# Optimization experiments

Hardware: AMD Instinct MI355X
Metric: run time of the kernel (lower is better)

Reference implementation:

```python
import jax, jax.numpy as jnp
import numpy as np
from jax import lax

LB, UB = 0.0, 0.1
N_ITERS = 32  # fixed-point iterations for water-filling rebalance


def _conv(x, w, b):
    y = lax.conv_general_dilated(x, w, (1, 1), ((1, 1), (1, 1)),
                                 dimension_numbers=("NCHW", "OIHW", "NCHW"))
    return y + b[None, :, None, None]


def _maxpool2(x):
    return lax.reduce_window(x, -jnp.inf, lax.max, (1, 1, 2, 2), (1, 1, 2, 2), "VALID")


def _linear(x, w, b):
    return x @ w.T + b


def _gru(x_num, W_ih, W_hh, b_ih, b_hh):
    # x_num: [B, S, N]; torch GRU gate order r, z, n
    B = x_num.shape[0]
    H = W_hh.shape[1]
    xs = jnp.swapaxes(x_num, 0, 1)  # [S, B, N]

    def step(h, x_t):
        gi = x_t @ W_ih.T + b_ih            # [B, 3H]
        gh = h @ W_hh.T + b_hh              # [B, 3H]
        i_r, i_z, i_n = jnp.split(gi, 3, axis=-1)
        h_r, h_z, h_n = jnp.split(gh, 3, axis=-1)
        r = jax.nn.sigmoid(i_r + h_r)
        z = jax.nn.sigmoid(i_z + h_z)
        n = jnp.tanh(i_n + r * h_n)
        h_new = (1.0 - z) * n + z * h
        return h_new, None

    h0 = jnp.zeros((B, H), dtype=x_num.dtype)
    h_last, _ = lax.scan(step, h0, xs)
    return h_last


def _rebalance_one(w):
    # vectorized fixed-point version of the per-sample while-loop water-filling
    def body(carry, _):
        old, wc = carry
        leftover = jnp.sum(old - wc)
        mask = wc != UB
        s = jnp.sum(jnp.where(mask, wc, 0.0))
        gift = jnp.where(mask & (s > 0), leftover * wc / jnp.where(s > 0, s, 1.0), 0.0)
        new_old = wc + gift
        new_wc = jnp.clip(new_old, LB, UB)
        return (new_old, new_wc), None

    init = (w, jnp.clip(w, LB, UB))
    (_, wc), _ = lax.scan(body, init, None, length=N_ITERS)
    return wc


def setup_inputs() -> dict:
    key = jax.random.key(0)
    ks = jax.random.split(key, 16)
    B, S, N, H_IMG, W_IMG, HID = 16, 60, 50, 64, 60, 128
    fc_in = 64 * (H_IMG // 4) * (W_IMG // 4)  # 15360
    sc = 0.05
    return {
        "x_num": jax.random.normal(ks[0], (B, S, N), jnp.float32),
        "x_img": jax.random.uniform(ks[1], (B, N, H_IMG, W_IMG), jnp.float32),
        "conv1_w": jax.random.normal(ks[2], (32, 1, 3, 3), jnp.float32) * sc,
        "conv1_b": jnp.zeros((32,), jnp.float32),
        "conv2_w": jax.random.normal(ks[3], (64, 32, 3, 3), jnp.float32) * sc,
        "conv2_b": jnp.zeros((64,), jnp.float32),
        "fc1_w": jax.random.normal(ks[4], (64, fc_in), jnp.float32) * 0.01,
        "fc1_b": jnp.zeros((64,), jnp.float32),
        "fc_binary_w": jax.random.normal(ks[5], (1, 64), jnp.float32) * sc,
        "fc_binary_b": jnp.zeros((1,), jnp.float32),
        "fc2_w": jax.random.normal(ks[6], (128, 64), jnp.float32) * sc,
        "fc2_b": jnp.zeros((128,), jnp.float32),
        "W_ih": jax.random.normal(ks[7], (3 * HID, N), jnp.float32) * sc,
        "W_hh": jax.random.normal(ks[8], (3 * HID, HID), jnp.float32) * sc,
        "b_ih": jnp.zeros((3 * HID,), jnp.float32),
        "b_hh": jnp.zeros((3 * HID,), jnp.float32),
        "gru_fc_w": jax.random.normal(ks[9], (N, HID), jnp.float32) * sc,
        "gru_fc_b": jnp.zeros((N,), jnp.float32),
        "fusion_w": jax.random.normal(ks[10], (64, N + 128), jnp.float32) * sc,
        "fusion_b": jnp.zeros((64,), jnp.float32),
        "final_w": jax.random.normal(ks[11], (N, 64), jnp.float32) * sc,
        "final_b": jnp.zeros((N,), jnp.float32),
    }


def reference(x_num, x_img, conv1_w, conv1_b, conv2_w, conv2_b, fc1_w, fc1_b,
              fc_binary_w, fc_binary_b, fc2_w, fc2_b, W_ih, W_hh, b_ih, b_hh,
              gru_fc_w, gru_fc_b, fusion_w, fusion_b, final_w, final_b):
    B, S, N = x_num.shape
    # GRU branch: last hidden -> Linear -> [B, N]
    h_last = _gru(x_num, W_ih, W_hh, b_ih, b_hh)
    numerical_features = _linear(h_last, gru_fc_w, gru_fc_b)

    # CNN branch on per-stock chart images
    xi = x_img.reshape(B * N, 1, x_img.shape[2], x_img.shape[3])
    h = _maxpool2(jax.nn.relu(_conv(xi, conv1_w, conv1_b)))
    h = _maxpool2(jax.nn.relu(_conv(h, conv2_w, conv2_b)))
    h = h.reshape(B * N, -1)
    feats = jax.nn.relu(_linear(h, fc1_w, fc1_b))
    binary_pred = jax.nn.sigmoid(_linear(feats, fc_binary_w, fc_binary_b))
    cnn_features = _linear(feats, fc2_w, fc2_b).reshape(B, N, -1).mean(axis=1)

    fused = jax.nn.relu(_linear(jnp.concatenate([numerical_features, cnn_features], axis=1), fusion_w, fusion_b))
    w = jax.nn.softmax(_linear(fused, final_w, final_b), axis=1)
    portfolio_weights = jax.vmap(_rebalance_one)(w)
    return portfolio_weights, binary_pred.reshape(B, N)
```

## Files before the change

kernel.cpp:

```cpp
#include <hip/hip_runtime.h>
#include <hip/hip_bf16.h>
#include <hip/hip_fp16.h>

typedef unsigned short ushort_t;
typedef short short8_t __attribute__((ext_vector_type(8)));
typedef _Float16 half8_t __attribute__((ext_vector_type(8)));
typedef _Float16 h2 __attribute__((ext_vector_type(2)));
typedef float f32x4 __attribute__((ext_vector_type(4)));
typedef float f32x16 __attribute__((ext_vector_type(16)));
typedef ushort_t us4_t __attribute__((ext_vector_type(4)));

#define NBATCH 16
#define SEQ    60
#define NSTK   50
#define HID    128
#define G3     384
#define NIMG   800
#define IH     64
#define IW     60
#define P1H    32
#define P1W    30
#define P2C    64
#define FCIN   15360

#define OFF_WHHF   0u
#define OFF_WPREP  24576u
#define OFF_WFC1   33792u
#define OFF_GI     525312u
#define OFF_HLAST  893952u
#define OFF_POOL2  896000u
#define OFF_FC2O   7040000u
#define OFF_PART   7142400u
#define OFF_W1H    7961600u
#define WS_FLOATS  7961760u

#define E_WHH  49152
#define E_WPR  18432
#define E_FC1  983040
#define E_W1H  160
#define E_TOT  (E_WHH + E_WPR + E_FC1 + E_W1H)

struct __align__(16) ConvS {
    ushort_t pool1t[18][4][32][8];
    union {
        float    imgp[35][60];
        ushort_t pool2s[64][120];
    } u;
};
struct __align__(16) GruS {
    float    gh[16 * 388];
    ushort_t hb[16 * 136];
};
#define SMEM_BYTES 52224

__device__ __forceinline__ float fast_sig(float x) {
    const float e = __expf(-x);
    return __builtin_amdgcn_rcpf(1.f + e);
}
__device__ __forceinline__ float fast_tanh(float x) {
    const float xc = fmaxf(fminf(x, 15.f), -15.f);
    const float e = __expf(2.f * xc);
    return (e - 1.f) * __builtin_amdgcn_rcpf(e + 1.f);
}
__device__ __forceinline__ h2 hmax2v(h2 a, h2 b) {
    h2 r;
    r[0] = a[0] > b[0] ? a[0] : b[0];
    r[1] = a[1] > b[1] ? a[1] : b[1];
    return r;
}

__global__ __launch_bounds__(384) void k_pre(const float* __restrict__ xnum,
                                             const float* __restrict__ wih,
                                             const float* __restrict__ bih,
                                             const float* __restrict__ whh,
                                             const float* __restrict__ c2w,
                                             const float* __restrict__ fc1w,
                                             const float* __restrict__ c1w,
                                             const float* __restrict__ c1b,
                                             float* __restrict__ GI,
                                             ushort_t* __restrict__ whhf,
                                             ushort_t* __restrict__ wprep,
                                             ushort_t* __restrict__ wfc1,
                                             unsigned int* __restrict__ w1h)
{
    const int bid = blockIdx.x;
    if (bid < 960) {
        const int s = bid >> 4, b = bid & 15;
        const int j = threadIdx.x;
        const float* xr = xnum + (size_t)(b * SEQ + s) * NSTK;
        const float* wr = wih + (size_t)j * NSTK;
        float a = bih[j];
        #pragma unroll 10
        for (int k = 0; k < NSTK; ++k) a = fmaf(xr[k], wr[k], a);
        GI[((size_t)s * 16 + b) * G3 + j] = a;
        return;
    }
    const int idx = (bid - 960) * 384 + threadIdx.x;
    if (idx < E_WHH) {
        const int e = idx;
        const int i = e & 7, l = (e >> 3) & 63, ksj = e >> 9;
        const int ks = ksj & 3, jt = ksj >> 2;
        const int j = jt * 16 + (l & 15);
        const int k = ks * 32 + ((l >> 4) << 3) + i;
        __hip_bfloat16 hv = __float2bfloat16(whh[j * HID + k]);
        whhf[e] = *(ushort_t*)&hv;
    } else if (idx < E_WHH + E_WPR) {
        const int e = idx - E_WHH;
        const int i = e & 7, l = (e >> 3) & 63, rest = e >> 9;
        const int ks = rest & 1, mt = rest >> 1;
        const int tap = mt % 9, mm = mt / 9;
        const int oc = mm * 32 + (l & 31);
        const int ic = ks * 16 + ((l >> 5) << 3) + i;
        const _Float16 hv = (_Float16)c2w[((size_t)oc * 32 + ic) * 9 + tap];
        wprep[e] = *(const ushort_t*)&hv;
    } else if (idx < E_WHH + E_WPR + E_FC1) {
        const int e = idx - (E_WHH + E_WPR);
        const int i = e & 7, l = (e >> 3) & 63, rest = e >> 9;
        const int n = rest & 3, T = rest >> 2;
        const int oc = n * 16 + (l & 15);
        const int k = T * 32 + ((l >> 4) << 3) + i;
        __hip_bfloat16 hv = __float2bfloat16(fc1w[(size_t)oc * FCIN + k]);
        wfc1[e] = *(ushort_t*)&hv;
    } else if (idx < E_TOT) {
        const int e = idx - (E_WHH + E_WPR + E_FC1);
        if (e < 144) {
            const int p = e / 9, tap = e - p * 9;
            const int ch0 = (p >> 2) * 8 + (p & 3) * 2;
            const _Float16 lo = (_Float16)c1w[ch0 * 9 + tap];
            const _Float16 hi = (_Float16)c1w[(ch0 + 1) * 9 + tap];
            w1h[p * 9 + tap] = ((unsigned)*(const ushort_t*)&hi << 16) | *(const ushort_t*)&lo;
        } else {
            const int p = e - 144;
            const int ch0 = (p >> 2) * 8 + (p & 3) * 2;
            const _Float16 lo = (_Float16)c1b[ch0];
            const _Float16 hi = (_Float16)c1b[ch0 + 1];
            w1h[144 + p] = ((unsigned)*(const ushort_t*)&hi << 16) | *(const ushort_t*)&lo;
        }
    }
}

__global__ __launch_bounds__(512, 3) void k_mega(const float* __restrict__ x_img,
                                                 const unsigned int* __restrict__ w1h,
                                                 const float* __restrict__ c2b,
                                                 const ushort_t* __restrict__ wprep,
                                                 const float* __restrict__ GI,
                                                 const ushort_t* __restrict__ whhf,
                                                 const float* __restrict__ bhh,
                                                 ushort_t* __restrict__ pool2,
                                                 float* __restrict__ hlast)
{
    extern __shared__ char smraw[];
    const int tid = threadIdx.x;
    const int bid = blockIdx.x;

    if (bid == 0) {
        GruS* g = (GruS*)smraw;
        const int w = tid >> 6, l = tid & 63;
        const int arow = l & 15, kq = l >> 4;
        short8_t wfr[3][4];
        #pragma unroll
        for (int jj = 0; jj < 3; ++jj)
            #pragma unroll
            for (int ks = 0; ks < 4; ++ks)
                wfr[jj][ks] = *(const short8_t*)&whhf[((((w * 3 + jj) * 4 + ks) * 64 + l) * 8)];

        const int b = tid >> 5, hh0 = (tid & 31) * 4;
        const f32x4 bhr = *(const f32x4*)&bhh[hh0];
        const f32x4 bhz = *(const f32x4*)&bhh[128 + hh0];
        const f32x4 bhn = *(const f32x4*)&bhh[256 + hh0];
        float h0 = 0.f, h1 = 0.f, h2v = 0.f, h3 = 0.f;
        for (int i = tid; i < 1088; i += 512) ((unsigned int*)g->hb)[i] = 0u;
        const float* gi0 = GI + b * G3 + hh0;
        f32x4 cr = *(const f32x4*)(gi0);
        f32x4 cz = *(const f32x4*)(gi0 + 128);
        f32x4 cn = *(const f32x4*)(gi0 + 256);
        __syncthreads();

        for (int s = 0; s < SEQ; ++s) {
            const int sn = (s + 1 < SEQ) ? s + 1 : s;
            const float* gnx = GI + ((size_t)sn * 16 + b) * G3 + hh0;
            const f32x4 nr = *(const f32x4*)(gnx);
            const f32x4 nz = *(const f32x4*)(gnx + 128);
            const f32x4 nn = *(const f32x4*)(gnx + 256);

            #pragma unroll
            for (int jj = 0; jj < 3; ++jj) {
                f32x4 a = {0.f, 0.f, 0.f, 0.f};
                #pragma unroll
                for (int ks = 0; ks < 4; ++ks) {
                    short8_t af = *(const short8_t*)&g->hb[arow * 136 + ks * 32 + kq * 8];
                    a = __builtin_amdgcn_mfma_f32_16x16x32_bf16(af, wfr[jj][ks], a, 0, 0, 0);
                }
                const int jt = w * 3 + jj;
                #pragma unroll
                for (int r = 0; r < 4; ++r)
                    g->gh[(kq * 4 + r) * 388 + jt * 16 + arow] = a[r];
            }
            __syncthreads();

            const f32x4 gr = *(const f32x4*)&g->gh[b * 388 + hh0];
            const f32x4 gz = *(const f32x4*)&g->gh[b * 388 + 128 + hh0];
            const f32x4 gn = *(const f32x4*)&g->gh[b * 388 + 256 + hh0];
            float hv0, hv1, hv2, hv3;
            {
                const float r0 = fast_sig(cr[0] + gr[0] + bhr[0]);
                const float z0 = fast_sig(cz[0] + gz[0] + bhz[0]);
                const float n0 = fast_tanh(cn[0] + r0 * (gn[0] + bhn[0]));
                hv0 = (1.f - z0) * n0 + z0 * h0;
                const float r1 = fast_sig(cr[1] + gr[1] + bhr[1]);
                const float z1 = fast_sig(cz[1] + gz[1] + bhz[1]);
                const float n1 = fast_tanh(cn[1] + r1 * (gn[1] + bhn[1]));
                hv1 = (1.f - z1) * n1 + z1 * h1;
                const float r2 = fast_sig(cr[2] + gr[2] + bhr[2]);
                const float z2 = fast_sig(cz[2] + gz[2] + bhz[2]);
                const float n2 = fast_tanh(cn[2] + r2 * (gn[2] + bhn[2]));
                hv2 = (1.f - z2) * n2 + z2 * h2v;
                const float r3 = fast_sig(cr[3] + gr[3] + bhr[3]);
                const float z3 = fast_sig(cz[3] + gz[3] + bhz[3]);
                const float n3 = fast_tanh(cn[3] + r3 * (gn[3] + bhn[3]));
                hv3 = (1.f - z3) * n3 + z3 * h3;
            }
            h0 = hv0; h1 = hv1; h2v = hv2; h3 = hv3;
            us4_t hp;
            { __hip_bfloat16 t0 = __float2bfloat16(h0);  hp[0] = *(ushort_t*)&t0; }
            { __hip_bfloat16 t1 = __float2bfloat16(h1);  hp[1] = *(ushort_t*)&t1; }
            { __hip_bfloat16 t2 = __float2bfloat16(h2v); hp[2] = *(ushort_t*)&t2; }
            { __hip_bfloat16 t3 = __float2bfloat16(h3);  hp[3] = *(ushort_t*)&t3; }
            *(us4_t*)&g->hb[b * 136 + hh0] = hp;
            cr = nr; cz = nz; cn = nn;
            __syncthreads();
        }
        f32x4 ho = {h0, h1, h2v, h3};
        *(f32x4*)&hlast[b * HID + hh0] = ho;
        return;
    }

    ConvS* c = (ConvS*)smraw;
    const int img  = (bid - 1) >> 1;
    const int half = (bid - 1) & 1;
    const float* xim = x_img + (size_t)img * (IH * IW);
    const int rowbase = 29 * half;

    {
        const short8_t z = {0, 0, 0, 0, 0, 0, 0, 0};
        const int zrow = half ? 17 : 0;
        if (tid < 128) {
            const int cg = tid >> 5, xs = tid & 31;
            *(short8_t*)&c->pool1t[zrow][cg][xs][0] = z;
        } else if (tid < 272) {
            const int q = tid - 128;
            const int ly = q / 8, cg = (q >> 1) & 3, xs = (q & 1) * 31;
            *(short8_t*)&c->pool1t[ly][cg][xs][0] = z;
        }
    }
    {
        const f32x4* src = (const f32x4*)(xim + rowbase * IW);
        f32x4* dst = (f32x4*)c->u.imgp;
        for (int i = tid; i < 525; i += 512) dst[i] = src[i];
    }
    __syncthreads();

    if (tid < 510) {
        const int gj = tid / 30, px = tid - gj * 30;
        const int g = half * 15 + gj;
        const int ly = gj + 1 - half;
        const h2 z2 = {(_Float16)0.f, (_Float16)0.f};
        h2 patch2[4][4];
        #pragma unroll
        for (int yy = 0; yy < 4; ++yy) {
            const int giy = 2 * g - 1 + yy;
            const int liy = giy - rowbase;
            #pragma unroll
            for (int xx = 0; xx < 4; ++xx) {
                const int ix = 2 * px - 1 + xx;
                const float v = (giy >= 0 && giy < IH && ix >= 0 && ix < IW)
                                    ? c->u.imgp[liy][ix] : 0.f;
                const _Float16 vh = (_Float16)v;
                h2 p2; p2[0] = vh; p2[1] = vh;
                patch2[yy][xx] = p2;
            }
        }
        #pragma unroll
        for (int cg = 0; cg < 4; ++cg) {
            unsigned int ov[4];
            #pragma unroll
            for (int pr = 0; pr < 4; ++pr) {
                const int p = cg * 4 + pr;
                h2 wv[9];
                #pragma unroll
                for (int t = 0; t < 9; ++t) {
                    const unsigned int wu = w1h[p * 9 + t];
                    wv[t] = *(const h2*)&wu;
                }
                h2 a00 = z2, a01 = z2, a10 = z2, a11 = z2;
                #pragma unroll
                for (int ky = 0; ky < 3; ++ky)
                    #pragma unroll
                    for (int kx = 0; kx < 3; ++kx) {
                        const h2 wt = wv[ky * 3 + kx];
                        a00 = wt * patch2[ky][kx]     + a00;
                        a01 = wt * patch2[ky][kx + 1] + a01;
                        a10 = wt * patch2[ky + 1][kx] + a10;
                        a11 = wt * patch2[ky + 1][kx + 1] + a11;
                    }
                const unsigned int bu = w1h[144 + p];
                const h2 bia2 = *(const h2*)&bu;
                h2 m = hmax2v(hmax2v(a00, a01), hmax2v(a10, a11));
                h2 r = hmax2v(m + bia2, z2);
                ov[pr] = *(unsigned int*)&r;
            }
            *(uint4*)&c->pool1t[ly][cg][px + 1][0] = *(uint4*)ov;
        }
    }
    __syncthreads();

    {
        const int w  = tid >> 6, l = tid & 63;
        const int m  = w & 1;
        const int hi = l >> 5;
        const int col = l & 31;

        half8_t af[9][2];
        #pragma unroll
        for (int tap = 0; tap < 9; ++tap)
            #pragma unroll
            for (int ks = 0; ks < 2; ++ks)
                af[tap][ks] = *(const half8_t*)&wprep[(((m * 9 + tap) * 2 + ks) * 64 + l) * 8];
        float bia[16];
        #pragma unroll
        for (int r = 0; r < 16; ++r)
            bia[r] = c2b[m * 32 + (r & 3) + 8 * (r >> 2) + 4 * hi];

        const bool wr = ((col & 1) == 0) && (col < 30);
        const int px = col >> 1;

        #pragma unroll
        for (int yy = 0; yy < 2; ++yy) {
            const int ypl = (w >> 1) + yy * 4;
            f32x16 a0, a1;
            #pragma unroll
            for (int r = 0; r < 16; ++r) { a0[r] = 0.f; a1[r] = 0.f; }
            #pragma unroll
            for (int ro = 0; ro < 4; ++ro) {
                const int ly = 2 * ypl + ro;
                half8_t bf[3][2];
                #pragma unroll
                for (int kx = 0; kx < 3; ++kx)
                    #pragma unroll
                    for (int ks = 0; ks < 2; ++ks)
                        bf[kx][ks] = *(const half8_t*)&c->pool1t[ly][ks * 2 + hi][kx + col][0];
                if (ro < 3) {
                    #pragma unroll
                    for (int kx = 0; kx < 3; ++kx)
                        #pragma unroll
                        for (int ks = 0; ks < 2; ++ks)
                            a0 = __builtin_amdgcn_mfma_f32_32x32x16_f16(af[ro * 3 + kx][ks], bf[kx][ks], a0, 0, 0, 0);
                }
                if (ro >= 1) {
                    #pragma unroll
                    for (int kx = 0; kx < 3; ++kx)
                        #pragma unroll
                        for (int ks = 0; ks < 2; ++ks)
                            a1 = __builtin_amdgcn_mfma_f32_32x32x16_f16(af[(ro - 1) * 3 + kx][ks], bf[kx][ks], a1, 0, 0, 0);
                }
            }
            #pragma unroll
            for (int r = 0; r < 16; ++r) {
                float v = fmaxf(a0[r], a1[r]);
                v = fmaxf(v, __shfl_xor(v, 1, 64));
                v = fmaxf(v + bia[r], 0.f);
                if (wr) {
                    const int oc = m * 32 + (r & 3) + 8 * (r >> 2) + 4 * hi;
                    __hip_bfloat16 hv = __float2bfloat16(v);
                    c->u.pool2s[oc][ypl * 15 + px] = *(ushort_t*)&hv;
                }
            }
        }
        __syncthreads();
        {
            int4* dst = (int4*)(pool2 + (size_t)img * FCIN);
            const int4* src = (const int4*)c->u.pool2s;
            #pragma unroll
            for (int jj = 0; jj < 2; ++jj) {
                const int i = tid + jj * 512;
                if (i < 960) {
                    const int oc = i / 15, cc = i - oc * 15;
                    dst[oc * 30 + half * 15 + cc] = src[i];
                }
            }
        }
    }
}

__global__ __launch_bounds__(256) void k_fc1(const ushort_t* __restrict__ pool2,
                                             const ushort_t* __restrict__ wfc1,
                                             float* __restrict__ part)
{
    const int mt = blockIdx.x >> 4;
    const int ks = blockIdx.x & 15;
    const int n = threadIdx.x >> 6, l = threadIdx.x & 63;
    const int arow = l & 15, kq = l >> 4;
    const int img16 = mt * 16;
    const ushort_t* Ab = pool2 + (size_t)(img16 + arow) * FCIN + ks * 960 + kq * 8;
    const ushort_t* Bb = wfc1 + ((size_t)(ks * 30 * 4 + n) * 64 + l) * 8;
    f32x4 acc0 = {0.f, 0.f, 0.f, 0.f}, acc1 = {0.f, 0.f, 0.f, 0.f};
    #pragma unroll 10
    for (int t = 0; t < 30; t += 2) {
        const short8_t aA = *(const short8_t*)(Ab + (size_t)t * 32);
        const short8_t bA = *(const short8_t*)(Bb + (size_t)t * 2048);
        const short8_t aB = *(const short8_t*)(Ab + (size_t)(t + 1) * 32);
        const short8_t bB = *(const short8_t*)(Bb + (size_t)(t + 1) * 2048);
        acc0 = __builtin_amdgcn_mfma_f32_16x16x32_bf16(aA, bA, acc0, 0, 0, 0);
        acc1 = __builtin_amdgcn_mfma_f32_16x16x32_bf16(aB, bB, acc1, 0, 0, 0);
    }
    float* dst = &part[((size_t)ks * NIMG + img16 + kq * 4) * 64 + n * 16 + arow];
    #pragma unroll
    for (int r = 0; r < 4; ++r)
        dst[(size_t)r * 64] = acc0[r] + acc1[r];
}

__device__ __forceinline__ float wave_sum(float v) {
    #pragma unroll
    for (int o = 32; o > 0; o >>= 1) v += __shfl_xor(v, o, 64);
    return v;
}
__device__ __forceinline__ float wave_max(float v) {
    #pragma unroll
    for (int o = 32; o > 0; o >>= 1) v = fmaxf(v, __shfl_xor(v, o, 64));
    return v;
}

__global__ __launch_bounds__(512) void k_post(const float* __restrict__ part,
                                              const float* __restrict__ fc1b,
                                              const float* __restrict__ fbw,
                                              const float* __restrict__ fbb,
                                              const float* __restrict__ fc2w,
                                              const float* __restrict__ fc2b,
                                              float* __restrict__ out,
                                              float* __restrict__ fc2o)
{
    const int t = threadIdx.x;
    const int im8 = t >> 6;
    const int tl = t & 63;
    const int img = blockIdx.x * 8 + im8;
    float s = fc1b[tl];
    #pragma unroll
    for (int ks = 0; ks < 16; ++ks) s += part[((size_t)ks * NIMG + img) * 64 + tl];
    const float f = fmaxf(s, 0.f);
    __shared__ float flc[8][64];
    flc[im8][tl] = f;
    const float bs = wave_sum(f * fbw[tl]);
    if (tl == 0) out[800 + img] = 1.f / (1.f + expf(-(bs + fbb[0])));
    __syncthreads();
    #pragma unroll
    for (int q = 0; q < 2; ++q) {
        const int j = tl + q * 64;
        float a2 = fc2b[j];
        #pragma unroll 8
        for (int k = 0; k < 64; ++k) a2 = fmaf(flc[im8][k], fc2w[j * 64 + k], a2);
        fc2o[(size_t)img * 128 + j] = a2;
    }
}

__global__ __launch_bounds__(64) void k_final(const float* __restrict__ hlast,
                                              const float* __restrict__ fc2o,
                                              const float* __restrict__ gw,
                                              const float* __restrict__ gb,
                                              const float* __restrict__ fw,
                                              const float* __restrict__ fb,
                                              const float* __restrict__ finw,
                                              const float* __restrict__ finb,
                                              float* __restrict__ out)
{
    const int b = blockIdx.x, t = threadIdx.x;
    __shared__ float cf[128], nf[64], fu[64];
    #pragma unroll
    for (int jj = 0; jj < 2; ++jj) {
        const int j = t + jj * 64;
        float s = 0.f;
        for (int n = 0; n < NSTK; ++n) s += fc2o[(size_t)(b * NSTK + n) * 128 + j];
        cf[j] = s * (1.0f / 50.0f);
    }
    float s = 0.f;
    if (t < NSTK) {
        s = gb[t];
        for (int k = 0; k < HID; ++k) s = fmaf(hlast[b * HID + k], gw[t * HID + k], s);
    }
    nf[t] = (t < NSTK) ? s : 0.f;
    __syncthreads();
    float f = fb[t];
    for (int k = 0; k < NSTK; ++k) f = fmaf(nf[k], fw[t * 178 + k], f);
    for (int k = 0; k < 128; ++k) f = fmaf(cf[k], fw[t * 178 + 50 + k], f);
    fu[t] = fmaxf(f, 0.f);
    __syncthreads();
    float L = -3.4e38f;
    if (t < NSTK) {
        L = finb[t];
        for (int k = 0; k < 64; ++k) L = fmaf(fu[k], finw[t * 64 + k], L);
    }
    const float m = wave_max(L);
    const float e = (t < NSTK) ? expf(L - m) : 0.f;
    const float se = wave_sum(e);
    const float wv = e / se;
    float old = wv;
    float wc = fminf(fmaxf(wv, 0.f), 0.1f);
    for (int it = 0; it < 32; ++it) {
        const float leftover = wave_sum(old - wc);
        const bool mask = (wc != 0.1f);
        const float ssum = wave_sum(mask ? wc : 0.f);
        const float gift = (mask && ssum > 0.f) ? leftover * wc / ssum : 0.f;
        old = wc + gift;
        wc = fminf(fmaxf(old, 0.f), 0.1f);
    }
    if (t < NSTK) out[b * NSTK + t] = wc;
}

extern "C" void kernel_launch(void* const* d_in, const int* in_sizes, int n_in,
                              void* d_out, int out_size, void* d_ws, size_t ws_size,
                              hipStream_t stream)
{
    const float* x_num = (const float*)d_in[0];
    const float* x_img = (const float*)d_in[1];
    const float* c1w  = (const float*)d_in[2];
    const float* c1b  = (const float*)d_in[3];
    const float* c2w  = (const float*)d_in[4];
    const float* c2b  = (const float*)d_in[5];
    const float* fc1w = (const float*)d_in[6];
    const float* fc1b = (const float*)d_in[7];
    const float* fbw  = (const float*)d_in[8];
    const float* fbb  = (const float*)d_in[9];
    const float* fc2w = (const float*)d_in[10];
    const float* fc2b = (const float*)d_in[11];
    const float* wih  = (const float*)d_in[12];
    const float* whh  = (const float*)d_in[13];
    const float* bih  = (const float*)d_in[14];
    const float* bhh  = (const float*)d_in[15];
    const float* gw   = (const float*)d_in[16];
    const float* gb   = (const float*)d_in[17];
    const float* fw   = (const float*)d_in[18];
    const float* fb   = (const float*)d_in[19];
    const float* finw = (const float*)d_in[20];
    const float* finb = (const float*)d_in[21];
    float* out = (float*)d_out;
    float* ws  = (float*)d_ws;
    if (ws_size < (size_t)WS_FLOATS * 4) return;

    ushort_t* whhf  = (ushort_t*)(ws + OFF_WHHF);
    ushort_t* wprep = (ushort_t*)(ws + OFF_WPREP);
    ushort_t* wfc1  = (ushort_t*)(ws + OFF_WFC1);
    float* GI       = ws + OFF_GI;
    float* hlast    = ws + OFF_HLAST;
    ushort_t* pool2 = (ushort_t*)(ws + OFF_POOL2);
    float* fc2o     = ws + OFF_FC2O;
    float* part     = ws + OFF_PART;
    unsigned int* w1h = (unsigned int*)(ws + OFF_W1H);

    (void)hipFuncSetAttribute(reinterpret_cast<const void*>(k_mega),
                              hipFuncAttributeMaxDynamicSharedMemorySize, SMEM_BYTES);

    k_pre   <<<960 + 2737, 384, 0, stream>>>(x_num, wih, bih, whh, c2w, fc1w, c1w, c1b,
                                             GI, whhf, wprep, wfc1, w1h);
    k_mega  <<<2 * NIMG + 1, 512, SMEM_BYTES, stream>>>(x_img, w1h, c2b, wprep,
                                                        GI, whhf, bhh, pool2, hlast);
    k_fc1   <<<50 * 16, 256, 0, stream>>>(pool2, wfc1, part);
    k_post  <<<100, 512, 0, stream>>>(part, fc1b, fbw, fbb, fc2w, fc2b, out, fc2o);
    k_final <<<NBATCH, 64, 0, stream>>>(hlast, fc2o, gw, gb, fw, fb, finw, finb, out);
}
```

Baseline: 146.1 us.

## Restructure GRU recurrence to compute gates from MFMA accumulators with double-buffered hidden state

```diff
diff --git a/kernel.cpp b/kernel.cpp
--- a/kernel.cpp
+++ b/kernel.cpp
@@ -8,7 +8,6 @@
 typedef _Float16 h2 __attribute__((ext_vector_type(2)));
 typedef float f32x4 __attribute__((ext_vector_type(4)));
 typedef float f32x16 __attribute__((ext_vector_type(16)));
-typedef ushort_t us4_t __attribute__((ext_vector_type(4)));
 
 #define NBATCH 16
 #define SEQ    60
@@ -48,8 +47,7 @@
     } u;
 };
 struct __align__(16) GruS {
-    float    gh[16 * 388];
-    ushort_t hb[16 * 136];
+    ushort_t hb[2][16 * 136];
 };
 #define SMEM_BYTES 52224
 
@@ -139,7 +137,7 @@
     }
 }
 
-__global__ __launch_bounds__(512, 3) void k_mega(const float* __restrict__ x_img,
+__global__ __launch_bounds__(512, 2) void k_mega(const float* __restrict__ x_img,
                                                  const unsigned int* __restrict__ w1h,
                                                  const float* __restrict__ c2b,
                                                  const ushort_t* __restrict__ wprep,
@@ -157,81 +155,56 @@
         GruS* g = (GruS*)smraw;
         const int w = tid >> 6, l = tid & 63;
         const int arow = l & 15, kq = l >> 4;
+        const int hh = w * 16 + (l & 15);
+        const int b0 = (l >> 4) * 4;
         short8_t wfr[3][4];
         #pragma unroll
-        for (int jj = 0; jj < 3; ++jj)
+        for (int g3 = 0; g3 < 3; ++g3)
             #pragma unroll
             for (int ks = 0; ks < 4; ++ks)
-                wfr[jj][ks] = *(const short8_t*)&whhf[((((w * 3 + jj) * 4 + ks) * 64 + l) * 8)];
-
-        const int b = tid >> 5, hh0 = (tid & 31) * 4;
-        const f32x4 bhr = *(const f32x4*)&bhh[hh0];
-        const f32x4 bhz = *(const f32x4*)&bhh[128 + hh0];
-        const f32x4 bhn = *(const f32x4*)&bhh[256 + hh0];
-        float h0 = 0.f, h1 = 0.f, h2v = 0.f, h3 = 0.f;
-        for (int i = tid; i < 1088; i += 512) ((unsigned int*)g->hb)[i] = 0u;
-        const float* gi0 = GI + b * G3 + hh0;
-        f32x4 cr = *(const f32x4*)(gi0);
-        f32x4 cz = *(const f32x4*)(gi0 + 128);
-        f32x4 cn = *(const f32x4*)(gi0 + 256);
+                wfr[g3][ks] = *(const short8_t*)&whhf[((((g3 * 8 + w) * 4 + ks) * 64 + l) * 8)];
+        const float bhr = bhh[hh];
+        const float bhz = bhh[128 + hh];
+        const float bhn = bhh[256 + hh];
+        float h[4] = {0.f, 0.f, 0.f, 0.f};
+        for (int i = tid; i < 1088; i += 512) ((unsigned int*)g->hb[0])[i] = 0u;
         __syncthreads();
 
+        int cur = 0;
         for (int s = 0; s < SEQ; ++s) {
-            const int sn = (s + 1 < SEQ) ? s + 1 : s;
-            const float* gnx = GI + ((size_t)sn * 16 + b) * G3 + hh0;
-            const f32x4 nr = *(const f32x4*)(gnx);
-            const f32x4 nz = *(const f32x4*)(gnx + 128);
-            const f32x4 nn = *(const f32x4*)(gnx + 256);
-
-            #pragma unroll
-            for (int jj = 0; jj < 3; ++jj) {
-                f32x4 a = {0.f, 0.f, 0.f, 0.f};
-                #pragma unroll
-                for (int ks = 0; ks < 4; ++ks) {
-                    short8_t af = *(const short8_t*)&g->hb[arow * 136 + ks * 32 + kq * 8];
-                    a = __builtin_amdgcn_mfma_f32_16x16x32_bf16(af, wfr[jj][ks], a, 0, 0, 0);
-                }
-                const int jt = w * 3 + jj;
-                #pragma unroll
-                for (int r = 0; r < 4; ++r)
-                    g->gh[(kq * 4 + r) * 388 + jt * 16 + arow] = a[r];
+            const float* gis = GI + ((size_t)s * 16 + b0) * G3 + hh;
+            float cr[4], cz[4], cn[4];
+            #pragma unroll
+            for (int r = 0; r < 4; ++r) {
+                cr[r] = gis[r * G3];
+                cz[r] = gis[r * G3 + 128];
+                cn[r] = gis[r * G3 + 256];
+            }
+            f32x4 ar = {0.f, 0.f, 0.f, 0.f};
+            f32x4 az = {0.f, 0.f, 0.f, 0.f};
+            f32x4 an = {0.f, 0.f, 0.f, 0.f};
+            #pragma unroll
+            for (int ks = 0; ks < 4; ++ks) {
+                const short8_t af = *(const short8_t*)&g->hb[cur][arow * 136 + ks * 32 + kq * 8];
+                ar = __builtin_amdgcn_mfma_f32_16x16x32_bf16(af, wfr[0][ks], ar, 0, 0, 0);
+                az = __builtin_amdgcn_mfma_f32_16x16x32_bf16(af, wfr[1][ks], az, 0, 0, 0);
+                an = __builtin_amdgcn_mfma_f32_16x16x32_bf16(af, wfr[2][ks], an, 0, 0, 0);
+            }
+            const int nxt = cur ^ 1;
+            #pragma unroll
+            for (int r = 0; r < 4; ++r) {
+                const float rg = fast_sig(cr[r] + ar[r] + bhr);
+                const float zg = fast_sig(cz[r] + az[r] + bhz);
+                const float ng = fast_tanh(cn[r] + rg * (an[r] + bhn));
+                h[r] = (1.f - zg) * ng + zg * h[r];
+                __hip_bfloat16 t = __float2bfloat16(h[r]);
+                g->hb[nxt][(b0 + r) * 136 + hh] = *(ushort_t*)&t;
             }
             __syncthreads();
-
-            const f32x4 gr = *(const f32x4*)&g->gh[b * 388 + hh0];
-            const f32x4 gz = *(const f32x4*)&g->gh[b * 388 + 128 + hh0];
-            const f32x4 gn = *(const f32x4*)&g->gh[b * 388 + 256 + hh0];
-            float hv0, hv1, hv2, hv3;
-            {
-                const float r0 = fast_sig(cr[0] + gr[0] + bhr[0]);
-                const float z0 = fast_sig(cz[0] + gz[0] + bhz[0]);
-                const float n0 = fast_tanh(cn[0] + r0 * (gn[0] + bhn[0]));
-                hv0 = (1.f - z0) * n0 + z0 * h0;
-                const float r1 = fast_sig(cr[1] + gr[1] + bhr[1]);
-                const float z1 = fast_sig(cz[1] + gz[1] + bhz[1]);
-                const float n1 = fast_tanh(cn[1] + r1 * (gn[1] + bhn[1]));
-                hv1 = (1.f - z1) * n1 + z1 * h1;
-                const float r2 = fast_sig(cr[2] + gr[2] + bhr[2]);
-                const float z2 = fast_sig(cz[2] + gz[2] + bhz[2]);
-                const float n2 = fast_tanh(cn[2] + r2 * (gn[2] + bhn[2]));
-                hv2 = (1.f - z2) * n2 + z2 * h2v;
-                const float r3 = fast_sig(cr[3] + gr[3] + bhr[3]);
-                const float z3 = fast_sig(cz[3] + gz[3] + bhz[3]);
-                const float n3 = fast_tanh(cn[3] + r3 * (gn[3] + bhn[3]));
-                hv3 = (1.f - z3) * n3 + z3 * h3;
-            }
-            h0 = hv0; h1 = hv1; h2v = hv2; h3 = hv3;
-            us4_t hp;
-            { __hip_bfloat16 t0 = __float2bfloat16(h0);  hp[0] = *(ushort_t*)&t0; }
-            { __hip_bfloat16 t1 = __float2bfloat16(h1);  hp[1] = *(ushort_t*)&t1; }
-            { __hip_bfloat16 t2 = __float2bfloat16(h2v); hp[2] = *(ushort_t*)&t2; }
-            { __hip_bfloat16 t3 = __float2bfloat16(h3);  hp[3] = *(ushort_t*)&t3; }
-            *(us4_t*)&g->hb[b * 136 + hh0] = hp;
-            cr = nr; cz = nz; cn = nn;
-            __syncthreads();
-        }
-        f32x4 ho = {h0, h1, h2v, h3};
-        *(f32x4*)&hlast[b * HID + hh0] = ho;
+            cur = nxt;
+        }
+        #pragma unroll
+        for (int r = 0; r < 4; ++r) hlast[(b0 + r) * HID + hh] = h[r];
         return;
     }
 
```

Measured after the change: 138.4 us. 1.06x faster.
